# Kernel optimization log

Hardware: AMD Instinct MI355X
Metric: run time of the kernel (lower is better)

Reference implementation:

```python
import jax, jax.numpy as jnp
import numpy as np

B, S, H, L = 8, 4096, 768, 256   # batch, seq_len, hidden_size, num_lines (= line_ids.max()+1)
ATT_HID = 1024                    # attention MLP hidden dim from nn.Linear(hidden,1024)


def setup_inputs() -> dict:
    key = jax.random.key(0)
    k0, k1, k2, k3 = jax.random.split(key, 4)
    token_hidden = jax.random.normal(k0, (B, S, H), dtype=jnp.float32)
    line_ids = jax.random.randint(k1, (B, S), 0, L)  # all valid; -1 would mark invalid
    W1 = jax.random.normal(k2, (H, ATT_HID), dtype=jnp.float32) * 0.02
    b1 = jnp.zeros((ATT_HID,), jnp.float32)
    W2 = jax.random.normal(k3, (ATT_HID, 1), dtype=jnp.float32) * 0.02
    b2 = jnp.zeros((1,), jnp.float32)
    return {"token_hidden": token_hidden, "line_ids": line_ids,
            "W1": W1, "b1": b1, "W2": W2, "b2": b2}


def reference(token_hidden, line_ids, W1, b1, W2, b2):
    b, s, h = token_hidden.shape
    num_lines = L
    n_seg = b * num_lines + 1  # last segment is a dump slot for invalid (-1) tokens

    # attention scores: Linear -> tanh -> Linear, squeeze(-1)  [b, s]
    scores = (jnp.tanh(token_hidden @ W1 + b1) @ W2 + b2)[..., 0]

    valid = (line_ids >= 0).reshape(-1)                                   # [b*s]
    seg = jnp.where(line_ids >= 0,
                    jnp.arange(b)[:, None] * num_lines + line_ids,
                    b * num_lines).reshape(-1)                            # [b*s]
    s_flat = jnp.where(valid, scores.reshape(-1), -jnp.inf)

    # segment-wise stable softmax
    m = jax.ops.segment_max(s_flat, seg, num_segments=n_seg)
    m = jnp.where(jnp.isfinite(m), m, 0.0)  # empty segments -> safe 0
    e = jnp.where(valid, jnp.exp(scores.reshape(-1) - m[seg]), 0.0)
    denom = jax.ops.segment_sum(e, seg, num_segments=n_seg)
    w = e / jnp.maximum(denom[seg], 1e-20)                                # [b*s]

    # weighted sum of tokens per (batch, line) segment
    feats = jax.ops.segment_sum(token_hidden.reshape(-1, h) * w[:, None],
                                seg, num_segments=n_seg)
    line_features = feats[: b * num_lines].reshape(b, num_lines, h)

    counts = jax.ops.segment_sum(valid.astype(jnp.float32), seg, num_segments=n_seg)
    line_mask = counts[: b * num_lines].reshape(b, num_lines) > 0
    return line_features, line_mask
```

## Files before the change

### kernel.cpp

```cpp
#include <hip/hip_runtime.h>
#include <hip/hip_bf16.h>
#include <string.h>

#define M_TOK 32768
#define H_DIM 768
#define AH    1024
#define NSEG  2048
#define NKT   12
#define XCONV_BLK 2048

typedef __attribute__((ext_vector_type(8))) __bf16 bf16x8;
typedef __attribute__((ext_vector_type(4))) float f32x4;

__device__ __forceinline__ float tanh_fast(float x) {
  float e = __expf(2.0f * x);
  return 1.0f - 2.0f * __builtin_amdgcn_rcpf(e + 1.0f);
}

__device__ __forceinline__ float bf2f(unsigned short u) {
  unsigned int v = (unsigned int)u << 16;
  float f;
  memcpy(&f, &v, 4);
  return f;
}

__global__ __launch_bounds__(256) void prep_kernel(
    const float* __restrict__ W1, __hip_bfloat16* __restrict__ W1t,
    const float4* __restrict__ X4, uint4* __restrict__ Xb4,
    const int* __restrict__ line_ids, int* __restrict__ sorted,
    int* __restrict__ offs, int* __restrict__ counts) {
  __shared__ float tile[32][33];
  __shared__ int hist[256];
  __shared__ int pfx[256];
  const int tid = threadIdx.x;
  if (blockIdx.x < 768) {
    int nt = blockIdx.x & 31, ktile = blockIdx.x >> 5;
    int n0 = nt * 32, k0 = ktile * 32;
    int tx = tid & 31, ty = tid >> 5;
    for (int r = ty; r < 32; r += 8)
      tile[r][tx] = W1[(size_t)(k0 + r) * AH + n0 + tx];
    __syncthreads();
    for (int r = ty; r < 32; r += 8)
      W1t[(size_t)(n0 + r) * H_DIM + k0 + tx] = __float2bfloat16(tile[tx][r]);
  } else if (blockIdx.x < 768 + XCONV_BLK) {
    const int i0 = (blockIdx.x - 768) * 256 + tid;
#pragma unroll
    for (int p = 0; p < 6; ++p) {
      const size_t i = (size_t)i0 + (size_t)p * (XCONV_BLK * 256);
      float4 v0 = X4[i * 2];
      float4 v1 = X4[i * 2 + 1];
      __hip_bfloat16 h[8] = {
          __float2bfloat16(v0.x), __float2bfloat16(v0.y),
          __float2bfloat16(v0.z), __float2bfloat16(v0.w),
          __float2bfloat16(v1.x), __float2bfloat16(v1.y),
          __float2bfloat16(v1.z), __float2bfloat16(v1.w)};
      uint4 pk;
      memcpy(&pk, h, 16);
      Xb4[i] = pk;
    }
  } else {
    const int bb = blockIdx.x - (768 + XCONV_BLK);
    const int base = bb * 4096;
    hist[tid] = 0;
    int ids[16];
#pragma unroll
    for (int c = 0; c < 16; ++c) ids[c] = line_ids[base + c * 256 + tid];
    __syncthreads();
#pragma unroll
    for (int c = 0; c < 16; ++c)
      if (ids[c] >= 0) atomicAdd(&hist[ids[c]], 1);
    __syncthreads();
    int v = hist[tid];
    pfx[tid] = v;
    __syncthreads();
    for (int d = 1; d < 256; d <<= 1) {
      int t = (tid >= d) ? pfx[tid - d] : 0;
      __syncthreads();
      pfx[tid] += t;
      __syncthreads();
    }
    int excl = pfx[tid] - v;
    counts[bb * 256 + tid] = v;
    offs[bb * 256 + tid] = excl;
    hist[tid] = excl;
    __syncthreads();
#pragma unroll
    for (int c = 0; c < 16; ++c) {
      int id = ids[c];
      if (id >= 0) {
        int p = atomicAdd(&hist[id], 1);
        sorted[base + p] = base + c * 256 + tid;
      }
    }
  }
}

#define WAITV(N) asm volatile("s_waitcnt vmcnt(" #N ")" ::: "memory")
#define WAITL0   asm volatile("s_waitcnt lgkmcnt(0)" ::: "memory")

__global__ __launch_bounds__(512, 2) void attn_score_kernel(
    const __hip_bfloat16* __restrict__ Xbg,
    const __hip_bfloat16* __restrict__ W1tg, const float* __restrict__ b1g,
    const float* __restrict__ W2g, float* __restrict__ scores2) {
  __shared__ __align__(16) __bf16 As[2][256 * 64];
  __shared__ __align__(16) __bf16 Bs[2][256 * 64];

  const int tid = threadIdx.x;
  const int bid = blockIdx.x;
  const int xcd = bid & 7;
  const int sq  = bid >> 3;
  const int m0  = (xcd * 16 + (sq >> 1)) * 256;
  const int np0 = (sq & 1) * 512;
  const int lane = tid & 63;
  const int wave = tid >> 6;
  const int wm   = wave >> 2;
  const int wx   = wave & 3;
  const int ml   = lane & 15;
  const int lh   = lane >> 4;

  const __bf16* Xb = (const __bf16*)Xbg;
  const __bf16* W  = (const __bf16*)W1tg;

  const int lr   = tid >> 3;
  const int scol = ((tid & 7) ^ (lr & 7)) << 3;

  int aRow[4], bRow[4];
#pragma unroll
  for (int q = 0; q < 4; ++q) {
    aRow[q] = m0 + ((q & 1) << 7) + ((q >> 1) << 6) + lr;
    int lrow = (q << 6) + lr;
    bRow[q] = np0 + (((lrow >> 5) & 3) << 6) + ((lrow >> 7) << 5) + (lrow & 31);
  }

  f32x4 acc[8][4];
#pragma unroll
  for (int i = 0; i < 8; ++i)
#pragma unroll
    for (int j = 0; j < 4; ++j) acc[i][j] = (f32x4)0.f;

  bf16x8 af[4][2], bfr[2][2];

  float b1v[2][4], w2v[2][4];
#pragma unroll
  for (int sd = 0; sd < 2; ++sd)
#pragma unroll
    for (int nf = 0; nf < 4; ++nf) {
      int n = np0 + sd * 256 + wx * 64 + nf * 16 + ml;
      b1v[sd][nf] = b1g[n];
      w2v[sd][nf] = W2g[n];
    }
  WAITV(0);

#define STAGE_A(q, buf, kt)                                                    \
  __builtin_amdgcn_global_load_lds(                                            \
      (const __attribute__((address_space(1))) void*)(Xb +                     \
          (size_t)aRow[q] * H_DIM + (kt) + scol),                              \
      (__attribute__((address_space(3))) void*)&As[buf][(q) * 4096 + tid * 8], \
      16, 0, 0)
#define STAGE_B(q, buf, kt, nsh)                                               \
  __builtin_amdgcn_global_load_lds(                                            \
      (const __attribute__((address_space(1))) void*)(W +                      \
          (size_t)(bRow[q] + (nsh)) * H_DIM + (kt) + scol),                    \
      (__attribute__((address_space(3))) void*)&Bs[buf][(q) * 4096 + tid * 8], \
      16, 0, 0)

#define DSRA(MH, P)                                                            \
  _Pragma("unroll") for (int lf = 0; lf < 4; ++lf) {                           \
    int ra = ((MH) << 7) + (wm << 6) + (lf << 4) + ml;                         \
    _Pragma("unroll") for (int kk = 0; kk < 2; ++kk) {                         \
      int ph = ((kk << 2) + lh) ^ (ml & 7);                                    \
      af[lf][kk] = *(const bf16x8*)&As[P][(ra << 6) + (ph << 3)];              \
    }                                                                          \
  }
#define DSRB(NH, P)                                                            \
  _Pragma("unroll") for (int jj = 0; jj < 2; ++jj) {                           \
    int rb = ((NH) << 7) + (wx << 5) + (jj << 4) + ml;                         \
    _Pragma("unroll") for (int kk = 0; kk < 2; ++kk) {                         \
      int ph = ((kk << 2) + lh) ^ (ml & 7);                                    \
      bfr[jj][kk] = *(const bf16x8*)&Bs[P][(rb << 6) + (ph << 3)];             \
    }                                                                          \
  }
#define MFMAQ(MH, NH)                                                          \
  __builtin_amdgcn_s_setprio(1);                                               \
  _Pragma("unroll") for (int kk = 0; kk < 2; ++kk)                             \
    _Pragma("unroll") for (int lf = 0; lf < 4; ++lf)                           \
      _Pragma("unroll") for (int jj = 0; jj < 2; ++jj)                         \
        acc[(MH) * 4 + lf][(NH) * 2 + jj] =                                    \
            __builtin_amdgcn_mfma_f32_16x16x32_bf16(                           \
                af[lf][kk], bfr[jj][kk], acc[(MH) * 4 + lf][(NH) * 2 + jj],    \
                0, 0, 0);                                                      \
  __builtin_amdgcn_s_setprio(0);

#define BARRIER __builtin_amdgcn_s_barrier()
#define SCHED0  __builtin_amdgcn_sched_barrier(0)

#define EPILOGUE(side)                                                         \
  {                                                                            \
    __syncthreads();                                                           \
    float* red = (float*)&As[1][0];                                            \
    _Pragma("unroll") for (int mf = 0; mf < 8; ++mf) {                         \
      _Pragma("unroll") for (int pp = 0; pp < 4; ++pp) {                       \
        float tsum = 0.f;                                                      \
        _Pragma("unroll") for (int nf = 0; nf < 4; ++nf)                       \
          tsum += tanh_fast(acc[mf][nf][pp] + b1v[side][nf]) * w2v[side][nf];  \
        tsum += __shfl_xor(tsum, 1);                                           \
        tsum += __shfl_xor(tsum, 2);                                           \
        tsum += __shfl_xor(tsum, 4);                                           \
        tsum += __shfl_xor(tsum, 8);                                           \
        if (ml == 0)                                                           \
          red[wx * 256 + wm * 128 + mf * 16 + lh * 4 + pp] = tsum;             \
      }                                                                        \
    }                                                                          \
    __syncthreads();                                                           \
    if (tid < 256) {                                                           \
      float v =                                                                \
          (red[tid] + red[256 + tid]) + (red[512 + tid] + red[768 + tid]);     \
      scores2[(size_t)(m0 + tid) * 4 + ((sq & 1) * 2 + (side))] = v;           \
    }                                                                          \
  }

  STAGE_A(0, 0, 0); STAGE_A(1, 0, 0);
  STAGE_B(0, 0, 0, 0); STAGE_B(1, 0, 0, 0);
  STAGE_A(2, 0, 0); STAGE_A(3, 0, 0);
  STAGE_B(2, 0, 0, 0); STAGE_B(3, 0, 0, 0);
  WAITV(4);
  BARRIER;

  int P = 0;
  for (int tt = 0; tt < 2 * NKT - 1; ++tt) {
    const int u   = tt + 1;
    const int ktu = ((u >= NKT) ? (u - NKT) : u) << 6;
    const int nsh = (u >= NKT) ? 256 : 0;

    DSRA(0, P); DSRB(0, P);
    STAGE_A(0, P ^ 1, ktu); STAGE_A(1, P ^ 1, ktu);
    asm volatile("s_waitcnt lgkmcnt(8)" ::: "memory");
    BARRIER;
    WAITL0; SCHED0;
    MFMAQ(0, 0);
    WAITV(4);
    BARRIER;

    DSRA(1, P);
    STAGE_B(0, P ^ 1, ktu, nsh); STAGE_B(1, P ^ 1, ktu, nsh);
    BARRIER;
    WAITL0; SCHED0;
    MFMAQ(1, 0);
    WAITV(4);
    BARRIER;

    DSRB(1, P);
    STAGE_A(2, P ^ 1, ktu); STAGE_A(3, P ^ 1, ktu);
    BARRIER;
    WAITL0; SCHED0;
    MFMAQ(1, 1);
    BARRIER;

    DSRA(0, P);
    STAGE_B(2, P ^ 1, ktu, nsh); STAGE_B(3, P ^ 1, ktu, nsh);
    BARRIER;
    WAITL0; SCHED0;
    MFMAQ(0, 1);
    WAITV(4);
    BARRIER;

    P ^= 1;

    if (tt == NKT - 1) {
      EPILOGUE(0);
#pragma unroll
      for (int i = 0; i < 8; ++i)
#pragma unroll
        for (int j = 0; j < 4; ++j) acc[i][j] = (f32x4)0.f;
      WAITV(0);
      __syncthreads();
    }
  }

  DSRA(0, 1); DSRB(0, 1);
  asm volatile("s_waitcnt lgkmcnt(8)" ::: "memory");
  BARRIER;
  WAITL0; SCHED0;
  MFMAQ(0, 0);
  WAITV(2);
  BARRIER;

  DSRA(1, 1);
  BARRIER;
  WAITL0; SCHED0;
  MFMAQ(1, 0);
  WAITV(0);
  BARRIER;

  DSRB(1, 1);
  BARRIER;
  WAITL0; SCHED0;
  MFMAQ(1, 1);
  BARRIER;

  DSRA(0, 1);
  BARRIER;
  WAITL0; SCHED0;
  MFMAQ(0, 1);

  EPILOGUE(1);
}

__global__ __launch_bounds__(256) void aggregate_kernel(
    const ushort* __restrict__ Xb, const float* __restrict__ scores2,
    const int* __restrict__ sorted, const int* __restrict__ offs,
    const int* __restrict__ counts, float4* __restrict__ out4,
    float* __restrict__ out_mask) {
  __shared__ int   tok[256];
  __shared__ float sw[256];
  __shared__ float wred[4];
  const int seg = blockIdx.x;
  const int b = seg >> 8;
  const int tid = threadIdx.x, lane = tid & 63, wave = tid >> 6;

  const int off = offs[seg];
  int cnt = counts[seg];
  if (cnt > 256) cnt = 256;
  if (tid == 0) out_mask[seg] = cnt > 0 ? 1.f : 0.f;
  if (cnt == 0) {
    if (tid < H_DIM / 4)
      out4[(size_t)seg * (H_DIM / 4) + tid] = make_float4(0.f, 0.f, 0.f, 0.f);
    return;
  }

  float lmax = -3.4e38f;
  if (tid < cnt) {
    int t = sorted[(b << 12) + off + tid];
    tok[tid] = t;
    const float4 a = *(const float4*)(scores2 + (size_t)t * 4);
    float sc = (a.x + a.y) + (a.z + a.w);
    sw[tid] = sc;
    lmax = sc;
  }
#pragma unroll
  for (int d = 1; d < 64; d <<= 1) lmax = fmaxf(lmax, __shfl_xor(lmax, d));
  if (lane == 0) wred[wave] = lmax;
  __syncthreads();
  float m = fmaxf(fmaxf(wred[0], wred[1]), fmaxf(wred[2], wred[3]));
  float lsum = 0.f;
  if (tid < cnt) {
    float e = __expf(sw[tid] - m);
    sw[tid] = e;
    lsum = e;
  }
#pragma unroll
  for (int d = 1; d < 64; d <<= 1) lsum += __shfl_xor(lsum, d);
  __syncthreads();
  if (lane == 0) wred[wave] = lsum;
  __syncthreads();
  float denom = wred[0] + wred[1] + wred[2] + wred[3];
  float inv = __builtin_amdgcn_rcpf(fmaxf(denom, 1e-20f));
  if (tid < cnt) sw[tid] *= inv;
  __syncthreads();
  if (tid < H_DIM / 4) {
    const ushort4* xb = (const ushort4*)Xb + tid;
    float4 acc = make_float4(0.f, 0.f, 0.f, 0.f);
    int t = 0;
    for (; t + 4 <= cnt; t += 4) {
      ushort4 u0 = xb[(size_t)tok[t]     * (H_DIM / 4)];
      ushort4 u1 = xb[(size_t)tok[t + 1] * (H_DIM / 4)];
      ushort4 u2 = xb[(size_t)tok[t + 2] * (H_DIM / 4)];
      ushort4 u3 = xb[(size_t)tok[t + 3] * (H_DIM / 4)];
      float w0 = sw[t], w1 = sw[t + 1], w2 = sw[t + 2], w3 = sw[t + 3];
      acc.x += w0 * bf2f(u0.x) + w1 * bf2f(u1.x) + w2 * bf2f(u2.x) + w3 * bf2f(u3.x);
      acc.y += w0 * bf2f(u0.y) + w1 * bf2f(u1.y) + w2 * bf2f(u2.y) + w3 * bf2f(u3.y);
      acc.z += w0 * bf2f(u0.z) + w1 * bf2f(u1.z) + w2 * bf2f(u2.z) + w3 * bf2f(u3.z);
      acc.w += w0 * bf2f(u0.w) + w1 * bf2f(u1.w) + w2 * bf2f(u2.w) + w3 * bf2f(u3.w);
    }
    for (; t < cnt; ++t) {
      ushort4 u = xb[(size_t)tok[t] * (H_DIM / 4)];
      float w = sw[t];
      acc.x += w * bf2f(u.x); acc.y += w * bf2f(u.y);
      acc.z += w * bf2f(u.z); acc.w += w * bf2f(u.w);
    }
    out4[(size_t)seg * (H_DIM / 4) + tid] = acc;
  }
}

extern "C" void kernel_launch(void* const* d_in, const int* in_sizes, int n_in,
                              void* d_out, int out_size, void* d_ws, size_t ws_size,
                              hipStream_t stream) {
  const float* X        = (const float*)d_in[0];
  const int*   line_ids = (const int*)d_in[1];
  const float* W1       = (const float*)d_in[2];
  const float* b1       = (const float*)d_in[3];
  const float* W2       = (const float*)d_in[4];

  char* p = (char*)d_ws;
  __hip_bfloat16* Xb      = (__hip_bfloat16*)p;  p += (size_t)M_TOK * H_DIM * 2;
  __hip_bfloat16* W1t     = (__hip_bfloat16*)p;  p += 1572864;
  float*          scores2 = (float*)p;           p += (size_t)M_TOK * 4 * 4;
  int*            sorted  = (int*)p;             p += (size_t)M_TOK * 4;
  int*            offs    = (int*)p;             p += (size_t)NSEG * 4;
  int*            counts  = (int*)p;             p += (size_t)NSEG * 4;

  float* out_feats = (float*)d_out;
  float* out_mask  = out_feats + (size_t)NSEG * H_DIM;

  prep_kernel<<<768 + XCONV_BLK + 8, 256, 0, stream>>>(
      W1, W1t, (const float4*)X, (uint4*)Xb, line_ids, sorted, offs, counts);
  attn_score_kernel<<<256, 512, 0, stream>>>(Xb, W1t, b1, W2, scores2);
  aggregate_kernel<<<NSEG, 256, 0, stream>>>((const ushort*)Xb, scores2,
                                             sorted, offs, counts,
                                             (float4*)out_feats, out_mask);
}
```

Baseline: 239.0 us.

## Retile attention GEMM to 128x256 tiles with W1 loaded directly to registers

The attention-score GEMM moves from 256 blocks of 512 threads (256x1024 output per block, both operands staged in LDS, deep hand-scheduled pipeline) to 1024 blocks of 256 threads. Each block now computes a 128x256 tile. Only X is staged through LDS, while each wave loads its W1 fragments straight from global memory into registers. The aim is better CU occupancy and load balance, and a simpler loop with less LDS traffic and fewer barriers. The trade-off is that W1 is no longer shared through LDS, so global and L2 traffic for W1 rises, and the fine-grained overlap of the old schedule is lost.

Measured after the change: 246.6 us. 3.2% more time.

```diff
diff --git a/kernel.cpp b/kernel.cpp
--- a/kernel.cpp
+++ b/kernel.cpp
@@ -96,25 +96,22 @@
 }
 
 #define WAITV(N) asm volatile("s_waitcnt vmcnt(" #N ")" ::: "memory")
-#define WAITL0   asm volatile("s_waitcnt lgkmcnt(0)" ::: "memory")
-
-__global__ __launch_bounds__(512, 2) void attn_score_kernel(
+
+__global__ __launch_bounds__(256, 2) void attn_score_kernel(
     const __hip_bfloat16* __restrict__ Xbg,
     const __hip_bfloat16* __restrict__ W1tg, const float* __restrict__ b1g,
     const float* __restrict__ W2g, float* __restrict__ scores2) {
-  __shared__ __align__(16) __bf16 As[2][256 * 64];
-  __shared__ __align__(16) __bf16 Bs[2][256 * 64];
-
-  const int tid = threadIdx.x;
-  const int bid = blockIdx.x;
-  const int xcd = bid & 7;
-  const int sq  = bid >> 3;
-  const int m0  = (xcd * 16 + (sq >> 1)) * 256;
-  const int np0 = (sq & 1) * 512;
+  __shared__ __align__(16) __bf16 As[2][128 * 64];
+
+  const int tid  = threadIdx.x;
+  const int bid  = blockIdx.x;
+  const int xcd  = bid & 7;
+  const int s    = bid >> 3;
+  const int m0   = (xcd * 32 + (s >> 2)) * 128;
+  const int ntl  = s & 3;
+  const int n0   = ntl * 256;
   const int lane = tid & 63;
-  const int wave = tid >> 6;
-  const int wm   = wave >> 2;
-  const int wx   = wave & 3;
+  const int wx   = tid >> 6;
   const int ml   = lane & 15;
   const int lh   = lane >> 4;
 
@@ -124,13 +121,12 @@
   const int lr   = tid >> 3;
   const int scol = ((tid & 7) ^ (lr & 7)) << 3;
 
-  int aRow[4], bRow[4];
-#pragma unroll
-  for (int q = 0; q < 4; ++q) {
-    aRow[q] = m0 + ((q & 1) << 7) + ((q >> 1) << 6) + lr;
-    int lrow = (q << 6) + lr;
-    bRow[q] = np0 + (((lrow >> 5) & 3) << 6) + ((lrow >> 7) << 5) + (lrow & 31);
-  }
+  int aRow[4];
+#pragma unroll
+  for (int q = 0; q < 4; ++q) aRow[q] = m0 + (q << 5) + lr;
+
+  const int nb = n0 + wx * 64 + ml;
+  const __bf16* Wl = W + (size_t)nb * H_DIM + lh * 8;
 
   f32x4 acc[8][4];
 #pragma unroll
@@ -138,172 +134,92 @@
 #pragma unroll
     for (int j = 0; j < 4; ++j) acc[i][j] = (f32x4)0.f;
 
-  bf16x8 af[4][2], bfr[2][2];
-
-  float b1v[2][4], w2v[2][4];
-#pragma unroll
-  for (int sd = 0; sd < 2; ++sd)
-#pragma unroll
-    for (int nf = 0; nf < 4; ++nf) {
-      int n = np0 + sd * 256 + wx * 64 + nf * 16 + ml;
-      b1v[sd][nf] = b1g[n];
-      w2v[sd][nf] = W2g[n];
-    }
-  WAITV(0);
+  float b1v[4], w2v[4];
+#pragma unroll
+  for (int nf = 0; nf < 4; ++nf) {
+    int n = nb + nf * 16;
+    b1v[nf] = b1g[n];
+    w2v[nf] = W2g[n];
+  }
 
 #define STAGE_A(q, buf, kt)                                                    \
   __builtin_amdgcn_global_load_lds(                                            \
       (const __attribute__((address_space(1))) void*)(Xb +                     \
           (size_t)aRow[q] * H_DIM + (kt) + scol),                              \
-      (__attribute__((address_space(3))) void*)&As[buf][(q) * 4096 + tid * 8], \
+      (__attribute__((address_space(3))) void*)&As[buf][(q) * 2048 + tid * 8], \
       16, 0, 0)
-#define STAGE_B(q, buf, kt, nsh)                                               \
-  __builtin_amdgcn_global_load_lds(                                            \
-      (const __attribute__((address_space(1))) void*)(W +                      \
-          (size_t)(bRow[q] + (nsh)) * H_DIM + (kt) + scol),                    \
-      (__attribute__((address_space(3))) void*)&Bs[buf][(q) * 4096 + tid * 8], \
-      16, 0, 0)
-
-#define DSRA(MH, P)                                                            \
-  _Pragma("unroll") for (int lf = 0; lf < 4; ++lf) {                           \
-    int ra = ((MH) << 7) + (wm << 6) + (lf << 4) + ml;                         \
-    _Pragma("unroll") for (int kk = 0; kk < 2; ++kk) {                         \
-      int ph = ((kk << 2) + lh) ^ (ml & 7);                                    \
-      af[lf][kk] = *(const bf16x8*)&As[P][(ra << 6) + (ph << 3)];              \
-    }                                                                          \
-  }
-#define DSRB(NH, P)                                                            \
-  _Pragma("unroll") for (int jj = 0; jj < 2; ++jj) {                           \
-    int rb = ((NH) << 7) + (wx << 5) + (jj << 4) + ml;                         \
-    _Pragma("unroll") for (int kk = 0; kk < 2; ++kk) {                         \
-      int ph = ((kk << 2) + lh) ^ (ml & 7);                                    \
-      bfr[jj][kk] = *(const bf16x8*)&Bs[P][(rb << 6) + (ph << 3)];             \
-    }                                                                          \
-  }
-#define MFMAQ(MH, NH)                                                          \
-  __builtin_amdgcn_s_setprio(1);                                               \
-  _Pragma("unroll") for (int kk = 0; kk < 2; ++kk)                             \
-    _Pragma("unroll") for (int lf = 0; lf < 4; ++lf)                           \
-      _Pragma("unroll") for (int jj = 0; jj < 2; ++jj)                         \
-        acc[(MH) * 4 + lf][(NH) * 2 + jj] =                                    \
-            __builtin_amdgcn_mfma_f32_16x16x32_bf16(                           \
-                af[lf][kk], bfr[jj][kk], acc[(MH) * 4 + lf][(NH) * 2 + jj],    \
-                0, 0, 0);                                                      \
-  __builtin_amdgcn_s_setprio(0);
-
-#define BARRIER __builtin_amdgcn_s_barrier()
-#define SCHED0  __builtin_amdgcn_sched_barrier(0)
-
-#define EPILOGUE(side)                                                         \
-  {                                                                            \
-    __syncthreads();                                                           \
-    float* red = (float*)&As[1][0];                                            \
-    _Pragma("unroll") for (int mf = 0; mf < 8; ++mf) {                         \
-      _Pragma("unroll") for (int pp = 0; pp < 4; ++pp) {                       \
-        float tsum = 0.f;                                                      \
-        _Pragma("unroll") for (int nf = 0; nf < 4; ++nf)                       \
-          tsum += tanh_fast(acc[mf][nf][pp] + b1v[side][nf]) * w2v[side][nf];  \
-        tsum += __shfl_xor(tsum, 1);                                           \
-        tsum += __shfl_xor(tsum, 2);                                           \
-        tsum += __shfl_xor(tsum, 4);                                           \
-        tsum += __shfl_xor(tsum, 8);                                           \
-        if (ml == 0)                                                           \
-          red[wx * 256 + wm * 128 + mf * 16 + lh * 4 + pp] = tsum;             \
-      }                                                                        \
-    }                                                                          \
-    __syncthreads();                                                           \
-    if (tid < 256) {                                                           \
-      float v =                                                                \
-          (red[tid] + red[256 + tid]) + (red[512 + tid] + red[768 + tid]);     \
-      scores2[(size_t)(m0 + tid) * 4 + ((sq & 1) * 2 + (side))] = v;           \
-    }                                                                          \
-  }
-
-  STAGE_A(0, 0, 0); STAGE_A(1, 0, 0);
-  STAGE_B(0, 0, 0, 0); STAGE_B(1, 0, 0, 0);
-  STAGE_A(2, 0, 0); STAGE_A(3, 0, 0);
-  STAGE_B(2, 0, 0, 0); STAGE_B(3, 0, 0, 0);
-  WAITV(4);
-  BARRIER;
-
-  int P = 0;
-  for (int tt = 0; tt < 2 * NKT - 1; ++tt) {
-    const int u   = tt + 1;
-    const int ktu = ((u >= NKT) ? (u - NKT) : u) << 6;
-    const int nsh = (u >= NKT) ? 256 : 0;
-
-    DSRA(0, P); DSRB(0, P);
-    STAGE_A(0, P ^ 1, ktu); STAGE_A(1, P ^ 1, ktu);
-    asm volatile("s_waitcnt lgkmcnt(8)" ::: "memory");
-    BARRIER;
-    WAITL0; SCHED0;
-    MFMAQ(0, 0);
-    WAITV(4);
-    BARRIER;
-
-    DSRA(1, P);
-    STAGE_B(0, P ^ 1, ktu, nsh); STAGE_B(1, P ^ 1, ktu, nsh);
-    BARRIER;
-    WAITL0; SCHED0;
-    MFMAQ(1, 0);
-    WAITV(4);
-    BARRIER;
-
-    DSRB(1, P);
-    STAGE_A(2, P ^ 1, ktu); STAGE_A(3, P ^ 1, ktu);
-    BARRIER;
-    WAITL0; SCHED0;
-    MFMAQ(1, 1);
-    BARRIER;
-
-    DSRA(0, P);
-    STAGE_B(2, P ^ 1, ktu, nsh); STAGE_B(3, P ^ 1, ktu, nsh);
-    BARRIER;
-    WAITL0; SCHED0;
-    MFMAQ(0, 1);
-    WAITV(4);
-    BARRIER;
-
-    P ^= 1;
-
-    if (tt == NKT - 1) {
-      EPILOGUE(0);
-#pragma unroll
-      for (int i = 0; i < 8; ++i)
-#pragma unroll
-        for (int j = 0; j < 4; ++j) acc[i][j] = (f32x4)0.f;
-      WAITV(0);
-      __syncthreads();
-    }
-  }
-
-  DSRA(0, 1); DSRB(0, 1);
-  asm volatile("s_waitcnt lgkmcnt(8)" ::: "memory");
-  BARRIER;
-  WAITL0; SCHED0;
-  MFMAQ(0, 0);
-  WAITV(2);
-  BARRIER;
-
-  DSRA(1, 1);
-  BARRIER;
-  WAITL0; SCHED0;
-  MFMAQ(1, 0);
+
+  STAGE_A(0, 0, 0); STAGE_A(1, 0, 0); STAGE_A(2, 0, 0); STAGE_A(3, 0, 0);
   WAITV(0);
-  BARRIER;
-
-  DSRB(1, 1);
-  BARRIER;
-  WAITL0; SCHED0;
-  MFMAQ(1, 1);
-  BARRIER;
-
-  DSRA(0, 1);
-  BARRIER;
-  WAITL0; SCHED0;
-  MFMAQ(0, 1);
-
-  EPILOGUE(1);
+  __builtin_amdgcn_s_barrier();
+
+  for (int t = 0; t < NKT; ++t) {
+    const int p  = t & 1;
+    const int kt = t << 6;
+
+    bf16x8 bfr[4][2];
+#pragma unroll
+    for (int nf = 0; nf < 4; ++nf)
+#pragma unroll
+      for (int kk = 0; kk < 2; ++kk)
+        bfr[nf][kk] =
+            *(const bf16x8*)(Wl + (size_t)(nf * 16) * H_DIM + kt + kk * 32);
+    __builtin_amdgcn_sched_barrier(0);
+    if (t < NKT - 1) {
+      STAGE_A(0, p ^ 1, kt + 64); STAGE_A(1, p ^ 1, kt + 64);
+      STAGE_A(2, p ^ 1, kt + 64); STAGE_A(3, p ^ 1, kt + 64);
+    }
+
+    bf16x8 af[4][2];
+#pragma unroll
+    for (int h = 0; h < 2; ++h) {
+#pragma unroll
+      for (int f = 0; f < 4; ++f) {
+        int ra = (h << 6) + (f << 4) + ml;
+#pragma unroll
+        for (int kk = 0; kk < 2; ++kk) {
+          int g = ((kk << 2) + lh) ^ (ml & 7);
+          af[f][kk] = *(const bf16x8*)&As[p][(ra << 6) + (g << 3)];
+        }
+      }
+      __builtin_amdgcn_s_setprio(1);
+#pragma unroll
+      for (int kk = 0; kk < 2; ++kk)
+#pragma unroll
+        for (int f = 0; f < 4; ++f)
+#pragma unroll
+          for (int nf = 0; nf < 4; ++nf)
+            acc[h * 4 + f][nf] = __builtin_amdgcn_mfma_f32_16x16x32_bf16(
+                af[f][kk], bfr[nf][kk], acc[h * 4 + f][nf], 0, 0, 0);
+      __builtin_amdgcn_s_setprio(0);
+    }
+    WAITV(0);
+    __builtin_amdgcn_s_barrier();
+  }
+
+  __syncthreads();
+  float* red = (float*)&As[0][0];
+#pragma unroll
+  for (int mf = 0; mf < 8; ++mf) {
+#pragma unroll
+    for (int pp = 0; pp < 4; ++pp) {
+      float tsum = 0.f;
+#pragma unroll
+      for (int nf = 0; nf < 4; ++nf)
+        tsum += tanh_fast(acc[mf][nf][pp] + b1v[nf]) * w2v[nf];
+      tsum += __shfl_xor(tsum, 1);
+      tsum += __shfl_xor(tsum, 2);
+      tsum += __shfl_xor(tsum, 4);
+      tsum += __shfl_xor(tsum, 8);
+      if (ml == 0)
+        red[wx * 128 + mf * 16 + lh * 4 + pp] = tsum;
+    }
+  }
+  __syncthreads();
+  if (tid < 128) {
+    float v = (red[tid] + red[128 + tid]) + (red[256 + tid] + red[384 + tid]);
+    scores2[(size_t)(m0 + tid) * 4 + ntl] = v;
+  }
 }
 
 __global__ __launch_bounds__(256) void aggregate_kernel(
@@ -404,7 +320,7 @@
 
   prep_kernel<<<768 + XCONV_BLK + 8, 256, 0, stream>>>(
       W1, W1t, (const float4*)X, (uint4*)Xb, line_ids, sorted, offs, counts);
-  attn_score_kernel<<<256, 512, 0, stream>>>(Xb, W1t, b1, W2, scores2);
+  attn_score_kernel<<<1024, 256, 0, stream>>>(Xb, W1t, b1, W2, scores2);
   aggregate_kernel<<<NSEG, 256, 0, stream>>>((const ushort*)Xb, scores2,
                                              sorted, offs, counts,
                                              (float4*)out_feats, out_mask);
```

## Double attention GEMM block to 1024 threads with simple double-buffered loop

Applied to the files above, without the earlier changes.

Reworks the attention-score GEMM kernel to launch 1024 threads (16 waves) per block. Each wave now computes a 64x64 output tile instead of 128x64. The hand-interleaved four-phase schedule with explicit vmcnt/lgkmcnt waits and split barriers is replaced by a plain loop that prefetches the next K-tile into the other buffer and synchronises once per iteration. b1/W2 loads move into the epilogue to save registers. The intent is to hide latency through more waves rather than manual scheduling, at the cost of less register-level operand reuse and more LDS reads per MFMA.

Result: no change. 234.5 us (-1.9%).

```diff
diff --git a/kernel.cpp b/kernel.cpp
--- a/kernel.cpp
+++ b/kernel.cpp
@@ -95,10 +95,7 @@
   }
 }
 
-#define WAITV(N) asm volatile("s_waitcnt vmcnt(" #N ")" ::: "memory")
-#define WAITL0   asm volatile("s_waitcnt lgkmcnt(0)" ::: "memory")
-
-__global__ __launch_bounds__(512, 2) void attn_score_kernel(
+__global__ __launch_bounds__(1024, 4) void attn_score_kernel(
     const __hip_bfloat16* __restrict__ Xbg,
     const __hip_bfloat16* __restrict__ W1tg, const float* __restrict__ b1g,
     const float* __restrict__ W2g, float* __restrict__ scores2) {
@@ -124,91 +121,46 @@
   const int lr   = tid >> 3;
   const int scol = ((tid & 7) ^ (lr & 7)) << 3;
 
-  int aRow[4], bRow[4];
-#pragma unroll
-  for (int q = 0; q < 4; ++q) {
-    aRow[q] = m0 + ((q & 1) << 7) + ((q >> 1) << 6) + lr;
-    int lrow = (q << 6) + lr;
-    bRow[q] = np0 + (((lrow >> 5) & 3) << 6) + ((lrow >> 7) << 5) + (lrow & 31);
-  }
-
-  f32x4 acc[8][4];
-#pragma unroll
-  for (int i = 0; i < 8; ++i)
+  f32x4 acc[4][4];
+#pragma unroll
+  for (int i = 0; i < 4; ++i)
 #pragma unroll
     for (int j = 0; j < 4; ++j) acc[i][j] = (f32x4)0.f;
-
-  bf16x8 af[4][2], bfr[2][2];
-
-  float b1v[2][4], w2v[2][4];
-#pragma unroll
-  for (int sd = 0; sd < 2; ++sd)
-#pragma unroll
-    for (int nf = 0; nf < 4; ++nf) {
-      int n = np0 + sd * 256 + wx * 64 + nf * 16 + ml;
-      b1v[sd][nf] = b1g[n];
-      w2v[sd][nf] = W2g[n];
-    }
-  WAITV(0);
 
 #define STAGE_A(q, buf, kt)                                                    \
   __builtin_amdgcn_global_load_lds(                                            \
       (const __attribute__((address_space(1))) void*)(Xb +                     \
-          (size_t)aRow[q] * H_DIM + (kt) + scol),                              \
-      (__attribute__((address_space(3))) void*)&As[buf][(q) * 4096 + tid * 8], \
+          (size_t)(m0 + (q) * 128 + lr) * H_DIM + (kt) + scol),                \
+      (__attribute__((address_space(3))) void*)&As[buf][(q) * 8192 + tid * 8], \
       16, 0, 0)
 #define STAGE_B(q, buf, kt, nsh)                                               \
   __builtin_amdgcn_global_load_lds(                                            \
       (const __attribute__((address_space(1))) void*)(W +                      \
-          (size_t)(bRow[q] + (nsh)) * H_DIM + (kt) + scol),                    \
-      (__attribute__((address_space(3))) void*)&Bs[buf][(q) * 4096 + tid * 8], \
+          (size_t)(np0 + (nsh) + (q) * 128 + lr) * H_DIM + (kt) + scol),       \
+      (__attribute__((address_space(3))) void*)&Bs[buf][(q) * 8192 + tid * 8], \
       16, 0, 0)
-
-#define DSRA(MH, P)                                                            \
-  _Pragma("unroll") for (int lf = 0; lf < 4; ++lf) {                           \
-    int ra = ((MH) << 7) + (wm << 6) + (lf << 4) + ml;                         \
-    _Pragma("unroll") for (int kk = 0; kk < 2; ++kk) {                         \
-      int ph = ((kk << 2) + lh) ^ (ml & 7);                                    \
-      af[lf][kk] = *(const bf16x8*)&As[P][(ra << 6) + (ph << 3)];              \
-    }                                                                          \
-  }
-#define DSRB(NH, P)                                                            \
-  _Pragma("unroll") for (int jj = 0; jj < 2; ++jj) {                           \
-    int rb = ((NH) << 7) + (wx << 5) + (jj << 4) + ml;                         \
-    _Pragma("unroll") for (int kk = 0; kk < 2; ++kk) {                         \
-      int ph = ((kk << 2) + lh) ^ (ml & 7);                                    \
-      bfr[jj][kk] = *(const bf16x8*)&Bs[P][(rb << 6) + (ph << 3)];             \
-    }                                                                          \
-  }
-#define MFMAQ(MH, NH)                                                          \
-  __builtin_amdgcn_s_setprio(1);                                               \
-  _Pragma("unroll") for (int kk = 0; kk < 2; ++kk)                             \
-    _Pragma("unroll") for (int lf = 0; lf < 4; ++lf)                           \
-      _Pragma("unroll") for (int jj = 0; jj < 2; ++jj)                         \
-        acc[(MH) * 4 + lf][(NH) * 2 + jj] =                                    \
-            __builtin_amdgcn_mfma_f32_16x16x32_bf16(                           \
-                af[lf][kk], bfr[jj][kk], acc[(MH) * 4 + lf][(NH) * 2 + jj],    \
-                0, 0, 0);                                                      \
-  __builtin_amdgcn_s_setprio(0);
-
-#define BARRIER __builtin_amdgcn_s_barrier()
-#define SCHED0  __builtin_amdgcn_sched_barrier(0)
 
 #define EPILOGUE(side)                                                         \
   {                                                                            \
     __syncthreads();                                                           \
     float* red = (float*)&As[1][0];                                            \
-    _Pragma("unroll") for (int mf = 0; mf < 8; ++mf) {                         \
+    float b1v[4], w2v[4];                                                      \
+    _Pragma("unroll") for (int nf = 0; nf < 4; ++nf) {                         \
+      int n = np0 + (side) * 256 + wx * 64 + nf * 16 + ml;                     \
+      b1v[nf] = b1g[n];                                                        \
+      w2v[nf] = W2g[n];                                                        \
+    }                                                                          \
+    _Pragma("unroll") for (int mf = 0; mf < 4; ++mf) {                         \
       _Pragma("unroll") for (int pp = 0; pp < 4; ++pp) {                       \
         float tsum = 0.f;                                                      \
         _Pragma("unroll") for (int nf = 0; nf < 4; ++nf)                       \
-          tsum += tanh_fast(acc[mf][nf][pp] + b1v[side][nf]) * w2v[side][nf];  \
+          tsum += tanh_fast(acc[mf][nf][pp] + b1v[nf]) * w2v[nf];              \
         tsum += __shfl_xor(tsum, 1);                                           \
         tsum += __shfl_xor(tsum, 2);                                           \
         tsum += __shfl_xor(tsum, 4);                                           \
         tsum += __shfl_xor(tsum, 8);                                           \
         if (ml == 0)                                                           \
-          red[wx * 256 + wm * 128 + mf * 16 + lh * 4 + pp] = tsum;             \
+          red[wx * 256 + wm * 64 + mf * 16 + lh * 4 + pp] = tsum;              \
       }                                                                        \
     }                                                                          \
     __syncthreads();                                                           \
@@ -217,91 +169,55 @@
           (red[tid] + red[256 + tid]) + (red[512 + tid] + red[768 + tid]);     \
       scores2[(size_t)(m0 + tid) * 4 + ((sq & 1) * 2 + (side))] = v;           \
     }                                                                          \
+    __syncthreads();                                                           \
   }
 
   STAGE_A(0, 0, 0); STAGE_A(1, 0, 0);
   STAGE_B(0, 0, 0, 0); STAGE_B(1, 0, 0, 0);
-  STAGE_A(2, 0, 0); STAGE_A(3, 0, 0);
-  STAGE_B(2, 0, 0, 0); STAGE_B(3, 0, 0, 0);
-  WAITV(4);
-  BARRIER;
-
-  int P = 0;
-  for (int tt = 0; tt < 2 * NKT - 1; ++tt) {
-    const int u   = tt + 1;
-    const int ktu = ((u >= NKT) ? (u - NKT) : u) << 6;
-    const int nsh = (u >= NKT) ? 256 : 0;
-
-    DSRA(0, P); DSRB(0, P);
-    STAGE_A(0, P ^ 1, ktu); STAGE_A(1, P ^ 1, ktu);
-    asm volatile("s_waitcnt lgkmcnt(8)" ::: "memory");
-    BARRIER;
-    WAITL0; SCHED0;
-    MFMAQ(0, 0);
-    WAITV(4);
-    BARRIER;
-
-    DSRA(1, P);
-    STAGE_B(0, P ^ 1, ktu, nsh); STAGE_B(1, P ^ 1, ktu, nsh);
-    BARRIER;
-    WAITL0; SCHED0;
-    MFMAQ(1, 0);
-    WAITV(4);
-    BARRIER;
-
-    DSRB(1, P);
-    STAGE_A(2, P ^ 1, ktu); STAGE_A(3, P ^ 1, ktu);
-    BARRIER;
-    WAITL0; SCHED0;
-    MFMAQ(1, 1);
-    BARRIER;
-
-    DSRA(0, P);
-    STAGE_B(2, P ^ 1, ktu, nsh); STAGE_B(3, P ^ 1, ktu, nsh);
-    BARRIER;
-    WAITL0; SCHED0;
-    MFMAQ(0, 1);
-    WAITV(4);
-    BARRIER;
-
-    P ^= 1;
+  __syncthreads();
+
+  for (int tt = 0; tt < 2 * NKT; ++tt) {
+    const int p = tt & 1;
+    if (tt < 2 * NKT - 1) {
+      const int u   = tt + 1;
+      const int ktu = ((u >= NKT) ? (u - NKT) : u) << 6;
+      const int nsh = (u >= NKT) ? 256 : 0;
+      STAGE_A(0, p ^ 1, ktu); STAGE_A(1, p ^ 1, ktu);
+      STAGE_B(0, p ^ 1, ktu, nsh); STAGE_B(1, p ^ 1, ktu, nsh);
+    }
+#pragma unroll
+    for (int kk = 0; kk < 2; ++kk) {
+      const int g = ((kk << 2) + lh) ^ (ml & 7);
+      bf16x8 af[4], bfv[4];
+#pragma unroll
+      for (int f = 0; f < 4; ++f) {
+        int ra = wm * 64 + f * 16 + ml;
+        af[f] = *(const bf16x8*)&As[p][(ra << 6) + (g << 3)];
+      }
+#pragma unroll
+      for (int nf = 0; nf < 4; ++nf) {
+        int rb = wx * 64 + nf * 16 + ml;
+        bfv[nf] = *(const bf16x8*)&Bs[p][(rb << 6) + (g << 3)];
+      }
+      __builtin_amdgcn_s_setprio(1);
+#pragma unroll
+      for (int f = 0; f < 4; ++f)
+#pragma unroll
+        for (int nf = 0; nf < 4; ++nf)
+          acc[f][nf] = __builtin_amdgcn_mfma_f32_16x16x32_bf16(
+              af[f], bfv[nf], acc[f][nf], 0, 0, 0);
+      __builtin_amdgcn_s_setprio(0);
+    }
+    __syncthreads();
 
     if (tt == NKT - 1) {
       EPILOGUE(0);
 #pragma unroll
-      for (int i = 0; i < 8; ++i)
+      for (int i = 0; i < 4; ++i)
 #pragma unroll
         for (int j = 0; j < 4; ++j) acc[i][j] = (f32x4)0.f;
-      WAITV(0);
-      __syncthreads();
-    }
-  }
-
-  DSRA(0, 1); DSRB(0, 1);
-  asm volatile("s_waitcnt lgkmcnt(8)" ::: "memory");
-  BARRIER;
-  WAITL0; SCHED0;
-  MFMAQ(0, 0);
-  WAITV(2);
-  BARRIER;
-
-  DSRA(1, 1);
-  BARRIER;
-  WAITL0; SCHED0;
-  MFMAQ(1, 0);
-  WAITV(0);
-  BARRIER;
-
-  DSRB(1, 1);
-  BARRIER;
-  WAITL0; SCHED0;
-  MFMAQ(1, 1);
-  BARRIER;
-
-  DSRA(0, 1);
-  BARRIER;
-  WAITL0; SCHED0;
-  MFMAQ(0, 1);
+    }
+  }
 
   EPILOGUE(1);
 }
@@ -404,7 +320,7 @@
 
   prep_kernel<<<768 + XCONV_BLK + 8, 256, 0, stream>>>(
       W1, W1t, (const float4*)X, (uint4*)Xb, line_ids, sorted, offs, counts);
-  attn_score_kernel<<<256, 512, 0, stream>>>(Xb, W1t, b1, W2, scores2);
+  attn_score_kernel<<<256, 1024, 0, stream>>>(Xb, W1t, b1, W2, scores2);
   aggregate_kernel<<<NSEG, 256, 0, stream>>>((const ushort*)Xb, scores2,
                                              sorted, offs, counts,
                                              (float4*)out_feats, out_mask);
```
